# Performance work log

Measured on AMD Instinct MI355X. Metric: run time of the kernel, lower is better.

## Reference

```python
import jax, jax.numpy as jnp
import numpy as np

B = 1024        # graphs per batch
NPG = 64        # nodes per graph (uniform)
DEG = 16        # avg degree
NE_PG = 256     # candidate non-edges per graph
N = B * NPG
E = N * DEG
NE = B * NE_PG
EMB, HID, NCAT, NET, NOUT = 64, 128, 100, 4, 101  # NOUT = num_external + 1


def setup_inputs() -> dict:
    key = jax.random.key(0)
    ks = jax.random.split(key, 32)
    rn = lambda k, shape: jax.random.normal(k, shape, jnp.float32) * 0.05
    # graph structure: edges and non-edges stay within each graph's node block
    x = jax.random.randint(ks[0], (N,), 0, NCAT)
    offs = jnp.repeat(jnp.arange(B) * NPG, NPG * DEG)
    src = jax.random.randint(ks[1], (E,), 0, NPG) + offs
    dst = jax.random.randint(ks[2], (E,), 0, NPG) + offs
    edge_index = jnp.stack([src, dst])
    edge_attr = jax.random.randint(ks[3], (E,), 0, NET)
    offs_ne = jnp.repeat(jnp.arange(B) * NPG, NE_PG)
    non_edges = jax.random.randint(ks[4], (NE, 2), 0, NPG) + offs_ne[:, None]
    batch = jnp.repeat(jnp.arange(B), NPG)
    return dict(
        node_tab=rn(ks[5], (NCAT, EMB)), edge_tab=rn(ks[6], (NET, EMB)),
        c1_w=rn(ks[7], (EMB, HID)), c1_we=rn(ks[8], (EMB, HID)),
        c1_as=rn(ks[9], (HID,)), c1_ad=rn(ks[10], (HID,)), c1_ae=rn(ks[11], (HID,)), c1_b=rn(ks[12], (HID,)),
        c2_w=rn(ks[13], (HID, HID)), c2_we=rn(ks[14], (EMB, HID)),
        c2_as=rn(ks[15], (HID,)), c2_ad=rn(ks[16], (HID,)), c2_ae=rn(ks[17], (HID,)), c2_b=rn(ks[18], (HID,)),
        s_w1=rn(ks[19], (HID, HID)), s_b1=rn(ks[20], (HID,)), s_w2=rn(ks[21], (HID, 1)), s_b2=rn(ks[22], (1,)),
        n_w1=rn(ks[23], (HID, HID)), n_b1=rn(ks[24], (HID,)), n_w2=rn(ks[25], (HID, NOUT)), n_b2=rn(ks[26], (NOUT,)),
        e_w1=rn(ks[27], (HID, HID)), e_b1=rn(ks[28], (HID,)), e_w2=rn(ks[29], (HID, 1)), e_b2=rn(ks[30], (1,)),
        x=x, edge_index=edge_index, edge_attr=edge_attr, non_edges=non_edges, batch=batch,
    )


def _gat(h_in, src, dst, e, W, We, a_s, a_d, a_e, b):
    """PyG GATConv, heads=1: gather -> leakyrelu logits -> segment softmax over dst -> scatter sum."""
    n = h_in.shape[0]
    h = h_in @ W                  # [N, C]
    he = e @ We                   # [E, C]
    logit = (h @ a_s)[src] + (h @ a_d)[dst] + he @ a_e   # [E]
    logit = jnp.where(logit > 0, logit, 0.2 * logit)      # leaky_relu(0.2)
    m = jax.ops.segment_max(logit, dst, num_segments=n)
    ex = jnp.exp(logit - m[dst])
    den = jax.ops.segment_sum(ex, dst, num_segments=n)
    alpha = ex / (den[dst] + 1e-16)
    return jax.ops.segment_sum(h[src] * alpha[:, None], dst, num_segments=n) + b


def _mlp(z, w1, b1, w2, b2):
    return jax.nn.relu(z @ w1 + b1) @ w2 + b2


def reference(node_tab, edge_tab,
              c1_w, c1_we, c1_as, c1_ad, c1_ae, c1_b,
              c2_w, c2_we, c2_as, c2_ad, c2_ae, c2_b,
              s_w1, s_b1, s_w2, s_b2,
              n_w1, n_b1, n_w2, n_b2,
              e_w1, e_b1, e_w2, e_b2,
              x, edge_index, edge_attr, non_edges, batch):
    src, dst = edge_index[0], edge_index[1]
    e = edge_tab[edge_attr]                      # [E, EMB]
    h = node_tab[x]                              # [N, EMB]
    h = jax.nn.relu(_gat(h, src, dst, e, c1_w, c1_we, c1_as, c1_ad, c1_ae, c1_b))
    h = _gat(h, src, dst, e, c2_w, c2_we, c2_as, c2_ad, c2_ae, c2_b)   # [N, HID]
    g = jax.ops.segment_sum(h, batch, num_segments=B)                   # [B, HID]
    stop = _mlp(g, s_w1, s_b1, s_w2, s_b2)                              # [B, 1]
    addnode = _mlp(h, n_w1, n_b1, n_w2, n_b2)                           # [N, NOUT]
    pair = h[non_edges[:, 0]] + h[non_edges[:, 1]]                      # [NE, HID]
    addedge = _mlp(pair, e_w1, e_b1, e_w2, e_b2)                        # [NE, 1]
    # uniform per-graph sizes -> the torch split/pad is a static reshape+concat
    return jnp.concatenate(
        [stop, addnode.reshape(B, NPG * NOUT), addedge.reshape(B, NE_PG)], axis=1)
```

## Files before the change

### kernel.cpp

```cpp
#include <hip/hip_runtime.h>
#include <hip/hip_bf16.h>


#define NPG 64
#define EPG 1024
#define NEPG 256
#define B_GR 1024
#define E_TOT 1048576
#define EMB 64
#define HID 128
#define NOUT 101
#define OUT_PG 6721

typedef __attribute__((ext_vector_type(8))) short bf16x8;
typedef __attribute__((ext_vector_type(4))) float f32x4;
typedef unsigned short ushort_t;

__device__ ushort_t g_nt1[100*HID];
__device__ ushort_t g_c2w[HID*HID];
__device__ ushort_t g_nw1[HID*HID];
__device__ ushort_t g_ew1[HID*HID];
__device__ ushort_t g_nw2[HID*112];
__device__ float    g_sw1t[HID*HID];
__device__ float    g_hs1[128], g_hd1[128];
__device__ float    g_he1[4], g_he2[4];

__device__ __forceinline__ ushort_t f2bf(float f) {
  unsigned u = __float_as_uint(f);
  return (ushort_t)((u + 0x7fffu + ((u >> 16) & 1u)) >> 16);
}
__device__ __forceinline__ float bf2f(ushort_t h) {
  return __uint_as_float(((unsigned)h) << 16);
}
__device__ __forceinline__ unsigned pk2(float a, float b) {
  __hip_bfloat162 h = __float22bfloat162_rn(make_float2(a, b));
  unsigned r; __builtin_memcpy(&r, &h, 4); return r;
}
__device__ __forceinline__ bf16x8 pk8(float4 v0, float4 v1) {
  union { bf16x8 v; unsigned u[4]; } o;
  o.u[0] = pk2(v0.x, v0.y); o.u[1] = pk2(v0.z, v0.w);
  o.u[2] = pk2(v1.x, v1.y); o.u[3] = pk2(v1.z, v1.w);
  return o.v;
}
__device__ __forceinline__ int pf_idx(int d, int s) {
  return d*64 + ((((s >> 2) ^ d) & 15) << 2) + (s & 3);
}

__global__ void prep_kernel(
    const float* __restrict__ node_tab, const float* __restrict__ edge_tab,
    const float* __restrict__ c1_w,  const float* __restrict__ c1_we,
    const float* __restrict__ c1_as, const float* __restrict__ c1_ad,
    const float* __restrict__ c1_ae,
    const float* __restrict__ c2_w,  const float* __restrict__ c2_we,
    const float* __restrict__ c2_ae,
    const float* __restrict__ s_w1,  const float* __restrict__ n_w1,
    const float* __restrict__ n_w2,  const float* __restrict__ e_w1)
{
  const int b = blockIdx.x, tid = threadIdx.x;
  if (b == 0) {
    __shared__ float v1[EMB], v2[EMB];
    if (tid < EMB) {
      float a = 0.f, d = 0.f;
      for (int j = 0; j < HID; ++j) {
        a = fmaf(c1_we[tid*HID + j], c1_ae[j], a);
        d = fmaf(c2_we[tid*HID + j], c2_ae[j], d);
      }
      v1[tid] = a; v2[tid] = d;
    }
    __syncthreads();
    if (tid < 4) {
      float a = 0.f, d = 0.f;
      for (int k = 0; k < EMB; ++k) {
        const float ev = edge_tab[tid*EMB + k];
        a = fmaf(ev, v1[k], a); d = fmaf(ev, v2[k], d);
      }
      g_he1[tid] = a; g_he2[tid] = d;
    }
    return;
  }
  if (b <= 50) {
    const int idx = (b - 1) * 256 + tid;
    const int i = idx >> 7, j = idx & (HID - 1);
    float s = 0.f;
    #pragma unroll 8
    for (int k = 0; k < EMB; ++k) s = fmaf(node_tab[i*EMB + k], c1_w[k*HID + j], s);
    g_nt1[idx] = f2bf(s);
    return;
  }
  if (b == 51) {
    __shared__ float vs[EMB], vd[EMB];
    if (tid < EMB) {
      float a = 0.f, d = 0.f;
      for (int j = 0; j < HID; ++j) {
        const float w = c1_w[tid*HID + j];
        a = fmaf(w, c1_as[j], a); d = fmaf(w, c1_ad[j], d);
      }
      vs[tid] = a; vd[tid] = d;
    }
    __syncthreads();
    if (tid < 128) {
      float a = 0.f, d = 0.f;
      if (tid < 100) {
        for (int k = 0; k < EMB; ++k) {
          const float xv = node_tab[tid*EMB + k];
          a = fmaf(xv, vs[k], a); d = fmaf(xv, vd[k], d);
        }
      }
      g_hs1[tid] = a; g_hd1[tid] = d;
    }
    return;
  }
  if (b <= 75) {
    const int grp = (b - 52) >> 3;
    const int chunk = (b - 52) & 7;
    const float* W = (grp == 0) ? c2_w : (grp == 1) ? n_w1 : e_w1;
    ushort_t* G = (grp == 0) ? g_c2w : (grp == 1) ? g_nw1 : g_ew1;
    const int base = chunk * 2048 + tid;
    #pragma unroll
    for (int it = 0; it < 8; ++it) {
      const int idx = base + it*256;
      const int j = idx & 7, l = (idx >> 3) & 63, r2 = idx >> 9;
      const int ks = r2 & 3, ct = r2 >> 2;
      const int row = ks*32 + (l >> 4)*8 + j;
      const int col = ct*16 + (l & 15);
      G[idx] = f2bf(W[row*HID + col]);
    }
    return;
  }
  if (b <= 82) {
    const int base = (b - 76) * 2048 + tid;
    #pragma unroll
    for (int it = 0; it < 8; ++it) {
      const int idx = base + it*256;
      const int j = idx & 7, l = (idx >> 3) & 63, r2 = idx >> 9;
      const int ks = r2 & 3, ct = r2 >> 2;
      const int row = ks*32 + (l >> 4)*8 + j;
      const int col = ct*16 + (l & 15);
      g_nw2[idx] = (col < NOUT) ? f2bf(n_w2[row*NOUT + col]) : (ushort_t)0;
    }
    return;
  }
  {
    const int base = (b - 83) * 2048 + tid;
    #pragma unroll
    for (int it = 0; it < 8; ++it) {
      const int idx = base + it*256;
      g_sw1t[idx] = s_w1[(idx & 127)*HID + (idx >> 7)];
    }
  }
}

#define S_HC   0
#define S_R    18432
#define S_PART 35840
#define S_NS   37888
#define S_ND   38144
#define S_GP   38400
#define S_EBW  38912
#define S_HCC  39936
#define S_XS   39968
#define S_TOT  40224

__global__ __launch_bounds__(512, 6) void graph_kernel(
    const float* __restrict__ c1_b,
    const float* __restrict__ c2_as, const float* __restrict__ c2_ad,
    const float* __restrict__ c2_b,
    const float* __restrict__ s_b1,  const float* __restrict__ s_w2,
    const float* __restrict__ s_b2,
    const float* __restrict__ n_b1,  const float* __restrict__ n_b2,
    const float* __restrict__ e_b1,  const float* __restrict__ e_w2,
    const float* __restrict__ e_b2,
    const int* __restrict__ x,  const int* __restrict__ ei,
    const int* __restrict__ ea, const int* __restrict__ nedg,
    float* __restrict__ out)
{
  const int tid = threadIdx.x;
  const int gid = blockIdx.x;
  const int nb = gid * NPG;
  const int lane = tid & 63;
  const int wv = tid >> 6;
  const int wr = wv & 3;
  const int ch = wv >> 2;
  const int qd = lane >> 4;
  const int cl = lane & 15;
  const int rb = wr * 16;

  __shared__ __align__(16) char smem[S_TOT];
  ushort_t* Hc   = (ushort_t*)(smem + S_HC);
  float*    Pf   = (float*)   (smem + S_R);
  ushort_t* Hr   = (ushort_t*)(smem + S_R);
  float*    part = (float*)   (smem + S_PART);
  float*    ns   = (float*)   (smem + S_NS);
  float*    nd   = (float*)   (smem + S_ND);
  float*    gp   = (float*)   (smem + S_GP);
  float*    ebw  = (float*)   (smem + S_EBW);
  float*    hc   = (float*)   (smem + S_HCC);
  int*      xs   = (int*)     (smem + S_XS);
  ushort_t* a1b  = Hc;

  unsigned er[2];
  #pragma unroll
  for (int i = 0; i < 2; ++i) {
    const int k = tid + 512*i;
    const int s = ei[gid*EPG + k] - nb;
    const int d = ei[E_TOT + gid*EPG + k] - nb;
    const int t = ea[gid*EPG + k];
    er[i] = (unsigned)(s | (d << 6) | (t << 12));
  }
  const int2 prr = *(const int2*)(nedg + 2*(gid*NEPG + (tid >> 1)));
  if (tid < NPG) {
    const int cat = x[nb + tid];
    xs[tid] = cat;
    ns[tid] = g_hs1[cat];
    nd[tid] = g_hd1[cat];
  }
  {
    float4* pz = (float4*)Pf;
    pz[tid]       = make_float4(0.f,0.f,0.f,0.f);
    pz[tid + 512] = make_float4(0.f,0.f,0.f,0.f);
  }
  if (tid < 128) gp[tid] = 0.f;
  if (tid < 256) ebw[tid] = (tid < 128) ? e_b1[tid] : e_w2[tid - 128];
  if (tid < 8) hc[tid] = (tid < 4) ? g_he1[tid] : g_he2[tid-4];
  __syncthreads();

  {
    const int f0 = wv * 16;
    const ushort_t* srcp = g_nt1 + xs[lane]*HID + f0;
    const bf16x8 t0 = ((const bf16x8*)srcp)[0];
    const bf16x8 t1 = ((const bf16x8*)srcp)[1];
    #pragma unroll
    for (int i = 0; i < 2; ++i) {
      const unsigned tp = er[i];
      const int s = tp & 63, d = (tp >> 6) & 63, t = tp >> 12;
      float l = ns[s] + nd[d] + hc[t];
      l = (l > 0.f) ? l : 0.2f * l;
      atomicAdd(&Pf[pf_idx(d, s)], __expf(l));
    }
    #pragma unroll
    for (int q = 0; q < 8; ++q) {
      Hc[(f0 +     q)*72 + lane] = (ushort_t)t0[q];
      Hc[(f0 + 8 + q)*72 + lane] = (ushort_t)t1[q];
    }
  }
  __syncthreads();

  bf16x8 pa0, pa1;
  float inv4[4];
  {
    const float* pr = Pf + (rb + cl)*64;
    const float4 v0 = *(const float4*)(pr + (((2*qd    ) ^ cl) << 2));
    const float4 v1 = *(const float4*)(pr + (((2*qd + 1) ^ cl) << 2));
    const float4 v2 = *(const float4*)(pr + (((2*qd + 8) ^ cl) << 2));
    const float4 v3 = *(const float4*)(pr + (((2*qd + 9) ^ cl) << 2));
    pa0 = pk8(v0, v1); pa1 = pk8(v2, v3);
    float den = v0.x+v0.y+v0.z+v0.w + v1.x+v1.y+v1.z+v1.w
              + v2.x+v2.y+v2.z+v2.w + v3.x+v3.y+v3.z+v3.w;
    den += __shfl_xor(den, 16, 64);
    den += __shfl_xor(den, 32, 64);
    #pragma unroll
    for (int r = 0; r < 4; ++r)
      inv4[r] = 1.f / (__shfl(den, qd*4 + r, 64) + 1e-16f);
  }
  if (tid < NPG) { ns[tid] = 0.f; nd[tid] = 0.f; }
  __syncthreads();

  {
    #pragma unroll
    for (int i = 0; i < 4; ++i) {
      const int ct = ch*4 + i;
      f32x4 acc = {0.f, 0.f, 0.f, 0.f};
      const bf16x8 b0 = *(const bf16x8*)(Hc + (ct*16+cl)*72 + qd*8);
      const bf16x8 b1 = *(const bf16x8*)(Hc + (ct*16+cl)*72 + 32 + qd*8);
      acc = __builtin_amdgcn_mfma_f32_16x16x32_bf16(pa0, b0, acc, 0, 0, 0);
      acc = __builtin_amdgcn_mfma_f32_16x16x32_bf16(pa1, b1, acc, 0, 0, 0);
      const int n = ct*16 + cl;
      const float bias = c1_b[n];
      #pragma unroll
      for (int r = 0; r < 4; ++r)
        Hr[(rb + qd*4 + r)*136 + n] = f2bf(fmaxf(fmaf(acc[r], inv4[r], bias), 0.f));
    }
  }
  __syncthreads();
  bf16x8 h1f[4];
  #pragma unroll
  for (int ks = 0; ks < 4; ++ks)
    h1f[ks] = *(const bf16x8*)(Hr + (rb+cl)*136 + ks*32 + qd*8);
  __syncthreads();

  {
    float4* pz = (float4*)Pf;
    pz[tid]       = make_float4(0.f,0.f,0.f,0.f);
    pz[tid + 512] = make_float4(0.f,0.f,0.f,0.f);
    float pns[4] = {0.f,0.f,0.f,0.f}, pnd[4] = {0.f,0.f,0.f,0.f};
    #pragma unroll
    for (int i = 0; i < 4; ++i) {
      const int ct = ch*4 + i;
      f32x4 acc = {0.f, 0.f, 0.f, 0.f};
      #pragma unroll
      for (int ks = 0; ks < 4; ++ks) {
        const bf16x8 b = *(const bf16x8*)(g_c2w + ((ct*4+ks)*64 + lane)*8);
        acc = __builtin_amdgcn_mfma_f32_16x16x32_bf16(h1f[ks], b, acc, 0, 0, 0);
      }
      const int n = ct*16 + cl;
      const float asv = c2_as[n], adv = c2_ad[n];
      uint2 pkd;
      pkd.x = pk2(acc[0], acc[1]);
      pkd.y = pk2(acc[2], acc[3]);
      *(uint2*)&Hc[n*72 + rb + qd*4] = pkd;
      #pragma unroll
      for (int r = 0; r < 4; ++r) {
        pns[r] = fmaf(acc[r], asv, pns[r]);
        pnd[r] = fmaf(acc[r], adv, pnd[r]);
      }
    }
    #pragma unroll
    for (int r = 0; r < 4; ++r) {
      #pragma unroll
      for (int off = 1; off < 16; off <<= 1) {
        pns[r] += __shfl_xor(pns[r], off, 64);
        pnd[r] += __shfl_xor(pnd[r], off, 64);
      }
    }
    if (cl == 0) {
      #pragma unroll
      for (int r = 0; r < 4; ++r) {
        atomicAdd(&ns[rb + qd*4 + r], pns[r]);
        atomicAdd(&nd[rb + qd*4 + r], pnd[r]);
      }
    }
  }
  __syncthreads();

  #pragma unroll
  for (int i = 0; i < 2; ++i) {
    const unsigned tp = er[i];
    const int s = tp & 63, d = (tp >> 6) & 63, t = tp >> 12;
    float l = ns[s] + nd[d] + hc[4 + t];
    l = (l > 0.f) ? l : 0.2f * l;
    atomicAdd(&Pf[pf_idx(d, s)], __expf(l));
  }
  __syncthreads();

  {
    const float* pr = Pf + (rb + cl)*64;
    const float4 v0 = *(const float4*)(pr + (((2*qd    ) ^ cl) << 2));
    const float4 v1 = *(const float4*)(pr + (((2*qd + 1) ^ cl) << 2));
    const float4 v2 = *(const float4*)(pr + (((2*qd + 8) ^ cl) << 2));
    const float4 v3 = *(const float4*)(pr + (((2*qd + 9) ^ cl) << 2));
    pa0 = pk8(v0, v1); pa1 = pk8(v2, v3);
    float den = v0.x+v0.y+v0.z+v0.w + v1.x+v1.y+v1.z+v1.w
              + v2.x+v2.y+v2.z+v2.w + v3.x+v3.y+v3.z+v3.w;
    den += __shfl_xor(den, 16, 64);
    den += __shfl_xor(den, 32, 64);
    #pragma unroll
    for (int r = 0; r < 4; ++r)
      inv4[r] = 1.f / (__shfl(den, qd*4 + r, 64) + 1e-16f);
  }
  __syncthreads();

  {
    #pragma unroll
    for (int i = 0; i < 4; ++i) {
      const int ct = ch*4 + i;
      f32x4 acc = {0.f, 0.f, 0.f, 0.f};
      const bf16x8 b0 = *(const bf16x8*)(Hc + (ct*16+cl)*72 + qd*8);
      const bf16x8 b1 = *(const bf16x8*)(Hc + (ct*16+cl)*72 + 32 + qd*8);
      acc = __builtin_amdgcn_mfma_f32_16x16x32_bf16(pa0, b0, acc, 0, 0, 0);
      acc = __builtin_amdgcn_mfma_f32_16x16x32_bf16(pa1, b1, acc, 0, 0, 0);
      const int n = ct*16 + cl;
      const float bias = c2_b[n];
      float colsum = 0.f;
      #pragma unroll
      for (int r = 0; r < 4; ++r) {
        const float v = fmaf(acc[r], inv4[r], bias);
        Hr[(rb + qd*4 + r)*136 + n] = f2bf(v);
        colsum += v;
      }
      colsum += __shfl_xor(colsum, 16, 64);
      colsum += __shfl_xor(colsum, 32, 64);
      if (qd == 0) atomicAdd(&gp[n], colsum);
    }
  }
  __syncthreads();

  {
    const int j = tid & 127, c = tid >> 7;
    const float* wrp = g_sw1t + j*HID + c*32;
    const float* grp = gp + c*32;
    float p = 0.f;
    #pragma unroll
    for (int q = 0; q < 8; ++q) {
      const float4 w = ((const float4*)wrp)[q];
      const float4 g = ((const float4*)grp)[q];
      p = fmaf(w.x, g.x, p); p = fmaf(w.y, g.y, p);
      p = fmaf(w.z, g.z, p); p = fmaf(w.w, g.w, p);
    }
    part[tid] = p;
  }
  bf16x8 h2f[4];
  #pragma unroll
  for (int ks = 0; ks < 4; ++ks)
    h2f[ks] = *(const bf16x8*)(Hr + (rb+cl)*136 + ks*32 + qd*8);
  __syncthreads();

  if (tid < 64) {
    const float d0 = part[tid]    + part[tid+128] + part[tid+256] + part[tid+384];
    const float d1 = part[tid+64] + part[tid+192] + part[tid+320] + part[tid+448];
    const float z0 = fmaxf(d0 + s_b1[tid], 0.f);
    const float z1 = fmaxf(d1 + s_b1[tid+64], 0.f);
    float p = fmaf(z0, s_w2[tid], z1 * s_w2[tid+64]);
    #pragma unroll
    for (int off = 32; off > 0; off >>= 1) p += __shfl_down(p, off, 64);
    if (tid == 0) out[(size_t)gid*OUT_PG] = p + s_b2[0];
  }

  {
    #pragma unroll
    for (int i = 0; i < 4; ++i) {
      const int ct = ch*4 + i;
      f32x4 an  = {0.f, 0.f, 0.f, 0.f};
      f32x4 ae2 = {0.f, 0.f, 0.f, 0.f};
      #pragma unroll
      for (int ks = 0; ks < 4; ++ks) {
        const bf16x8 bn = *(const bf16x8*)(g_nw1 + ((ct*4+ks)*64 + lane)*8);
        const bf16x8 be = *(const bf16x8*)(g_ew1 + ((ct*4+ks)*64 + lane)*8);
        an  = __builtin_amdgcn_mfma_f32_16x16x32_bf16(h2f[ks], bn, an, 0, 0, 0);
        ae2 = __builtin_amdgcn_mfma_f32_16x16x32_bf16(h2f[ks], be, ae2, 0, 0, 0);
      }
      const int n = ct*16 + cl;
      const float bias = n_b1[n];
      #pragma unroll
      for (int r = 0; r < 4; ++r) {
        a1b[(rb + qd*4 + r)*136 + n] = f2bf(fmaxf(an[r] + bias, 0.f));
        Hr[(rb + qd*4 + r)*136 + n] = f2bf(ae2[r]);
      }
    }
  }
  __syncthreads();

  {
    const int pi = tid >> 1, hf = tid & 1;
    const ushort_t* ui = Hr + (prr.x - nb)*136 + hf*64;
    const ushort_t* uj = Hr + (prr.y - nb)*136 + hf*64;
    float ssum = 0.f;
    #pragma unroll
    for (int q8 = 0; q8 < 8; ++q8) {
      const bf16x8 va = *(const bf16x8*)(ui + q8*8);
      const bf16x8 vb = *(const bf16x8*)(uj + q8*8);
      #pragma unroll
      for (int j = 0; j < 8; ++j) {
        const int c = hf*64 + q8*8 + j;
        float v = bf2f((ushort_t)va[j]) + bf2f((ushort_t)vb[j]) + ebw[c];
        v = fmaxf(v, 0.f);
        ssum = fmaf(v, ebw[128 + c], ssum);
      }
    }
    ssum += __shfl_xor(ssum, 1, 64);
    if (hf == 0)
      out[(size_t)gid*OUT_PG + 1 + NPG*NOUT + pi] = ssum + e_b2[0];
  }

  {
    bf16x8 af[4];
    #pragma unroll
    for (int ks = 0; ks < 4; ++ks)
      af[ks] = *(const bf16x8*)(a1b + (rb+cl)*136 + ks*32 + qd*8);
    float* ob = out + (size_t)gid*OUT_PG + 1;
    #pragma unroll
    for (int i = 0; i < 4; ++i) {
      const int ct = ch*4 + i;
      if (ct < 7) {
        f32x4 acc = {0.f, 0.f, 0.f, 0.f};
        #pragma unroll
        for (int ks = 0; ks < 4; ++ks) {
          const bf16x8 b = *(const bf16x8*)(g_nw2 + ((ct*4+ks)*64 + lane)*8);
          acc = __builtin_amdgcn_mfma_f32_16x16x32_bf16(af[ks], b, acc, 0, 0, 0);
        }
        const int o = ct*16 + cl;
        if (o < NOUT) {
          const float b2 = n_b2[o];
          #pragma unroll
          for (int r = 0; r < 4; ++r)
            ob[(size_t)(rb + qd*4 + r)*NOUT + o] = acc[r] + b2;
        }
      }
    }
  }
}

extern "C" void kernel_launch(void* const* d_in, const int* in_sizes, int n_in,
                              void* d_out, int out_size, void* d_ws, size_t ws_size,
                              hipStream_t stream) {
  const float* node_tab = (const float*)d_in[0];
  const float* edge_tab = (const float*)d_in[1];
  const float* c1_w  = (const float*)d_in[2];
  const float* c1_we = (const float*)d_in[3];
  const float* c1_as = (const float*)d_in[4];
  const float* c1_ad = (const float*)d_in[5];
  const float* c1_ae = (const float*)d_in[6];
  const float* c1_b  = (const float*)d_in[7];
  const float* c2_w  = (const float*)d_in[8];
  const float* c2_we = (const float*)d_in[9];
  const float* c2_as = (const float*)d_in[10];
  const float* c2_ad = (const float*)d_in[11];
  const float* c2_ae = (const float*)d_in[12];
  const float* c2_b  = (const float*)d_in[13];
  const float* s_w1  = (const float*)d_in[14];
  const float* s_b1  = (const float*)d_in[15];
  const float* s_w2  = (const float*)d_in[16];
  const float* s_b2  = (const float*)d_in[17];
  const float* n_w1  = (const float*)d_in[18];
  const float* n_b1  = (const float*)d_in[19];
  const float* n_w2  = (const float*)d_in[20];
  const float* n_b2  = (const float*)d_in[21];
  const float* e_w1  = (const float*)d_in[22];
  const float* e_b1  = (const float*)d_in[23];
  const float* e_w2  = (const float*)d_in[24];
  const float* e_b2  = (const float*)d_in[25];
  const int* x    = (const int*)d_in[26];
  const int* ei   = (const int*)d_in[27];
  const int* ea   = (const int*)d_in[28];
  const int* nedg = (const int*)d_in[29];
  float* out = (float*)d_out;

  prep_kernel<<<dim3(91), dim3(256), 0, stream>>>(
      node_tab, edge_tab, c1_w, c1_we, c1_as, c1_ad, c1_ae,
      c2_w, c2_we, c2_ae, s_w1, n_w1, n_w2, e_w1);

  graph_kernel<<<dim3(B_GR), dim3(512), 0, stream>>>(
      c1_b, c2_as, c2_ad, c2_b, s_b1, s_w2, s_b2,
      n_b1, n_b2, e_b1, e_w2, e_b2, x, ei, ea, nedg, out);
}
```

Before: 190.5 us.

## Split Pf and Hr LDS regions to drop barriers; use LDS-only waitcnt barriers

Gives the attention-probability buffer and the hidden-row buffer separate shared-memory regions, so several block-wide barriers that guarded their reuse are removed. Barriers are replaced with a custom barrier that waits only on LDS counters, not global memory, so outstanding global loads and stores need not drain at each sync. The ebw load moves later into the freed Pf region. Shared memory grows from about 40 KB to 53.5 KB per block, which may cut resident blocks per CU, and the custom barrier relies on global reads not being needed across barriers.

```diff
diff --git a/kernel.cpp b/kernel.cpp
--- a/kernel.cpp
+++ b/kernel.cpp
@@ -44,6 +44,11 @@
 }
 __device__ __forceinline__ int pf_idx(int d, int s) {
   return d*64 + ((((s >> 2) ^ d) & 15) << 2) + (s & 3);
+}
+__device__ __forceinline__ void bar_lds() {
+  asm volatile("s_waitcnt lgkmcnt(0)" ::: "memory");
+  __builtin_amdgcn_s_barrier();
+  asm volatile("" ::: "memory");
 }
 
 __global__ void prep_kernel(
@@ -151,15 +156,14 @@
 }
 
 #define S_HC   0
-#define S_R    18432
-#define S_PART 35840
-#define S_NS   37888
-#define S_ND   38144
-#define S_GP   38400
-#define S_EBW  38912
-#define S_HCC  39936
-#define S_XS   39968
-#define S_TOT  40224
+#define S_PF   18432
+#define S_HR   34816
+#define S_NS   52224
+#define S_ND   52480
+#define S_GP   52736
+#define S_HCC  53248
+#define S_XS   53280
+#define S_TOT  53536
 
 __global__ __launch_bounds__(512, 6) void graph_kernel(
     const float* __restrict__ c1_b,
@@ -187,13 +191,13 @@
 
   __shared__ __align__(16) char smem[S_TOT];
   ushort_t* Hc   = (ushort_t*)(smem + S_HC);
-  float*    Pf   = (float*)   (smem + S_R);
-  ushort_t* Hr   = (ushort_t*)(smem + S_R);
-  float*    part = (float*)   (smem + S_PART);
+  float*    Pf   = (float*)   (smem + S_PF);
+  ushort_t* Hr   = (ushort_t*)(smem + S_HR);
+  float*    part = (float*)   (smem + S_PF);
+  float*    ebw  = (float*)   (smem + S_PF + 2048);
   float*    ns   = (float*)   (smem + S_NS);
   float*    nd   = (float*)   (smem + S_ND);
   float*    gp   = (float*)   (smem + S_GP);
-  float*    ebw  = (float*)   (smem + S_EBW);
   float*    hc   = (float*)   (smem + S_HCC);
   int*      xs   = (int*)     (smem + S_XS);
   ushort_t* a1b  = Hc;
@@ -220,9 +224,8 @@
     pz[tid + 512] = make_float4(0.f,0.f,0.f,0.f);
   }
   if (tid < 128) gp[tid] = 0.f;
-  if (tid < 256) ebw[tid] = (tid < 128) ? e_b1[tid] : e_w2[tid - 128];
   if (tid < 8) hc[tid] = (tid < 4) ? g_he1[tid] : g_he2[tid-4];
-  __syncthreads();
+  bar_lds();
 
   {
     const int f0 = wv * 16;
@@ -243,11 +246,11 @@
       Hc[(f0 + 8 + q)*72 + lane] = (ushort_t)t1[q];
     }
   }
-  __syncthreads();
-
-  bf16x8 pa0, pa1;
-  float inv4[4];
-  {
+  bar_lds();
+
+  {
+    bf16x8 pa0, pa1;
+    float inv4[4];
     const float* pr = Pf + (rb + cl)*64;
     const float4 v0 = *(const float4*)(pr + (((2*qd    ) ^ cl) << 2));
     const float4 v1 = *(const float4*)(pr + (((2*qd + 1) ^ cl) << 2));
@@ -261,11 +264,7 @@
     #pragma unroll
     for (int r = 0; r < 4; ++r)
       inv4[r] = 1.f / (__shfl(den, qd*4 + r, 64) + 1e-16f);
-  }
-  if (tid < NPG) { ns[tid] = 0.f; nd[tid] = 0.f; }
-  __syncthreads();
-
-  {
+    if (tid < NPG) { ns[tid] = 0.f; nd[tid] = 0.f; }
     #pragma unroll
     for (int i = 0; i < 4; ++i) {
       const int ct = ch*4 + i;
@@ -281,14 +280,13 @@
         Hr[(rb + qd*4 + r)*136 + n] = f2bf(fmaxf(fmaf(acc[r], inv4[r], bias), 0.f));
     }
   }
-  __syncthreads();
-  bf16x8 h1f[4];
-  #pragma unroll
-  for (int ks = 0; ks < 4; ++ks)
-    h1f[ks] = *(const bf16x8*)(Hr + (rb+cl)*136 + ks*32 + qd*8);
-  __syncthreads();
-
-  {
+  bar_lds();
+
+  {
+    bf16x8 h1f[4];
+    #pragma unroll
+    for (int ks = 0; ks < 4; ++ks)
+      h1f[ks] = *(const bf16x8*)(Hr + (rb+cl)*136 + ks*32 + qd*8);
     float4* pz = (float4*)Pf;
     pz[tid]       = make_float4(0.f,0.f,0.f,0.f);
     pz[tid + 512] = make_float4(0.f,0.f,0.f,0.f);
@@ -330,7 +328,7 @@
       }
     }
   }
-  __syncthreads();
+  bar_lds();
 
   #pragma unroll
   for (int i = 0; i < 2; ++i) {
@@ -340,9 +338,11 @@
     l = (l > 0.f) ? l : 0.2f * l;
     atomicAdd(&Pf[pf_idx(d, s)], __expf(l));
   }
-  __syncthreads();
-
-  {
+  bar_lds();
+
+  {
+    bf16x8 pa0, pa1;
+    float inv4[4];
     const float* pr = Pf + (rb + cl)*64;
     const float4 v0 = *(const float4*)(pr + (((2*qd    ) ^ cl) << 2));
     const float4 v1 = *(const float4*)(pr + (((2*qd + 1) ^ cl) << 2));
@@ -356,10 +356,6 @@
     #pragma unroll
     for (int r = 0; r < 4; ++r)
       inv4[r] = 1.f / (__shfl(den, qd*4 + r, 64) + 1e-16f);
-  }
-  __syncthreads();
-
-  {
     #pragma unroll
     for (int i = 0; i < 4; ++i) {
       const int ct = ch*4 + i;
@@ -382,7 +378,7 @@
       if (qd == 0) atomicAdd(&gp[n], colsum);
     }
   }
-  __syncthreads();
+  bar_lds();
 
   {
     const int j = tid & 127, c = tid >> 7;
@@ -398,11 +394,12 @@
     }
     part[tid] = p;
   }
+  if (tid < 256) ebw[tid] = (tid < 128) ? e_b1[tid] : e_w2[tid - 128];
   bf16x8 h2f[4];
   #pragma unroll
   for (int ks = 0; ks < 4; ++ks)
     h2f[ks] = *(const bf16x8*)(Hr + (rb+cl)*136 + ks*32 + qd*8);
-  __syncthreads();
+  bar_lds();
 
   if (tid < 64) {
     const float d0 = part[tid]    + part[tid+128] + part[tid+256] + part[tid+384];
@@ -414,7 +411,6 @@
     for (int off = 32; off > 0; off >>= 1) p += __shfl_down(p, off, 64);
     if (tid == 0) out[(size_t)gid*OUT_PG] = p + s_b2[0];
   }
-
   {
     #pragma unroll
     for (int i = 0; i < 4; ++i) {
@@ -437,7 +433,7 @@
       }
     }
   }
-  __syncthreads();
+  bar_lds();
 
   {
     const int pi = tid >> 1, hf = tid & 1;
@@ -460,7 +456,6 @@
     if (hf == 0)
       out[(size_t)gid*OUT_PG + 1 + NPG*NOUT + pi] = ssum + e_b2[0];
   }
-
   {
     bf16x8 af[4];
     #pragma unroll
```

New measurement: 190.0 us. Within noise of the previous version (-0.2%).
